# Optimization experiments

Hardware: AMD Instinct MI355X
Metric: run time of the kernel (lower is better)

Reference implementation:

```python
import jax, jax.numpy as jnp
import numpy as np

LAYERS, STACKS, K = 10, 3, 2
DILATIONS = [2 ** i for _ in range(STACKS) for i in range(LAYERS)]  # 30 layers


def conv1d(x, w, b=None, dilation=1):
    # x: [N, C_in, T], w: [C_out, C_in, K] (torch Conv1d layout), VALID padding
    out = jax.lax.conv_general_dilated(
        x, w, window_strides=(1,), padding='VALID',
        rhs_dilation=(dilation,), dimension_numbers=('NCH', 'OIH', 'NCH'))
    if b is not None:
        out = out + b[None, :, None]
    return out


def setup_inputs() -> dict:
    key = jax.random.key(0)
    ks = jax.random.split(key, 12)
    s = 0.1  # weight scale to avoid gate saturation
    return {
        'y': jax.random.normal(ks[0], (16, 1, 16384), dtype=jnp.float32),
        'causal_w': jax.random.normal(ks[1], (32, 1, 1), dtype=jnp.float32) * s,
        'causal_b': jax.random.normal(ks[2], (32,), dtype=jnp.float32) * s,
        'filt_w': jax.random.normal(ks[3], (30, 32, 32, K), dtype=jnp.float32) * s,
        'gate_w': jax.random.normal(ks[4], (30, 32, 32, K), dtype=jnp.float32) * s,
        'res_w': jax.random.normal(ks[5], (30, 32, 32, 1), dtype=jnp.float32) * s,
        'skip_w': jax.random.normal(ks[6], (30, 256, 32, 1), dtype=jnp.float32) * s,
        'end1_w': jax.random.normal(ks[7], (256, 256, 1), dtype=jnp.float32) * s,
        'end1_b': jax.random.normal(ks[8], (256,), dtype=jnp.float32) * s,
        'end2_w': jax.random.normal(ks[9], (256, 256, 1), dtype=jnp.float32) * s,
        'end2_b': jax.random.normal(ks[10], (256,), dtype=jnp.float32) * s,
    }


def reference(y, causal_w, causal_b, filt_w, gate_w, res_w, skip_w,
              end1_w, end1_b, end2_w, end2_b):
    x = conv1d(y, causal_w, causal_b)  # [B, 32, T]
    skip = None
    for i, d in enumerate(DILATIONS):
        r = x
        f = jnp.tanh(conv1d(x, filt_w[i], dilation=d))      # [B,32,T-d]
        g = jax.nn.sigmoid(conv1d(x, gate_w[i], dilation=d))
        x = f * g
        s = conv1d(x, skip_w[i])                             # [B,256,T-d]
        t = s.shape[-1]
        skip = s if skip is None else s + skip[:, :, -t:]
        x = conv1d(x, res_w[i])
        x = x + r[:, :, -x.shape[-1]:]
    x = jax.nn.relu(skip)
    x = jax.nn.relu(conv1d(x, end1_w, end1_b))
    x = conv1d(x, end2_w, end2_b)
    return x
```

## Files before the change

kernel.cpp:

```cpp
#include <hip/hip_runtime.h>
#include <hip/hip_bf16.h>
#include <cstdint>

#define NB 16
#define NC 32
#define T0 16384
#define NL 30
#define SKC 256
#define TF 13315
#define WGRP 192
#define XBC 320
#define XBS 20

typedef _Float16 f16;
typedef _Float16 f16x2 __attribute__((ext_vector_type(2)));
typedef _Float16 f16x8 __attribute__((ext_vector_type(8)));
typedef float f32x4 __attribute__((ext_vector_type(4)));
typedef uint32_t u32;

#define MFMA16(a,b,c) __builtin_amdgcn_mfma_f32_16x16x32_f16(a,b,c,0,0,0)

#define SCF (-2.88539008f)
#define SCG (-1.44269504f)
#define CLF 86.6f
#define CLG 43.3f

__device__ __forceinline__ float frcp(float x){
#if __has_builtin(__builtin_amdgcn_rcpf)
  return __builtin_amdgcn_rcpf(x);
#else
  return 1.f/x;
#endif
}
__device__ __forceinline__ float fexp2(float x){
#if __has_builtin(__builtin_amdgcn_exp2f)
  return __builtin_amdgcn_exp2f(x);
#else
  return exp2f(x);
#endif
}
__device__ __forceinline__ float clampf(float x, float c){
#if __has_builtin(__builtin_amdgcn_fmed3f)
  return __builtin_amdgcn_fmed3f(x, -c, c);
#else
  return fminf(fmaxf(x, -c), c);
#endif
}
__device__ __forceinline__ u32 pk2(float x, float y){
#if __has_builtin(__builtin_amdgcn_cvt_pkrtz)
  return __builtin_bit_cast(u32, __builtin_amdgcn_cvt_pkrtz(x, y));
#else
  f16x2 r; r.x = (f16)x; r.y = (f16)y;
  return __builtin_bit_cast(u32, r);
#endif
}
__device__ __forceinline__ u32 pkadd(u32 a, u32 b){
  f16x2 s = __builtin_bit_cast(f16x2, a) + __builtin_bit_cast(f16x2, b);
  return __builtin_bit_cast(u32, s);
}
__device__ __forceinline__ size_t zfrag_off(int lz, int q){
  return (size_t)(lz & ~63)*NC + (size_t)(((lz>>4)&3)*512 + (q*16 + (lz&15))*8);
}
__device__ __forceinline__ int sigma_co(int q, int j){
  return (j < 4) ? (4*q + j) : (12 + 4*q + j);
}

__global__ __launch_bounds__(256) void prep3(
    const float* __restrict__ sw, const float* __restrict__ e1w,
    const float* __restrict__ e2w, const float* __restrict__ fw,
    const float* __restrict__ gw, const float* __restrict__ rw,
    f16* __restrict__ wsk, f16* __restrict__ e1f, f16* __restrict__ e2f,
    f16* __restrict__ fgpf, f16* __restrict__ ggpf, u32* __restrict__ rwp){
  int idx = blockIdx.x*256 + threadIdx.x;
  if (idx < 30720){
    int lane = idx & 63, mt = (idx>>6)&15, i = idx>>10;
    int m = mt*16 + (lane&15);
    int q = lane >> 4;
    const float* s = sw + ((size_t)i*SKC + m)*NC;
    f16* dp = wsk + (size_t)idx*8;
    #pragma unroll
    for (int j=0;j<8;j++) dp[j] = (f16)s[sigma_co(q, j)];
  } else if (idx < 38912){
    int j2 = idx - 30720;
    int lane = j2&63, mt = (j2>>6)&15, ks = j2>>10;
    int m = mt*16 + (lane&15);
    int k = ks*32 + (lane>>4)*8;
    const float* s = e1w + (size_t)m*SKC + k;
    f16* dp = e1f + (size_t)j2*8;
    #pragma unroll
    for (int j=0;j<8;j++) dp[j] = (f16)s[j];
  } else if (idx < 47104){
    int j2 = idx - 38912;
    int lane = j2&63, mt = (j2>>6)&15, ks = j2>>10;
    int m = mt*16 + (lane&15);
    int k = ks*32 + (lane>>4)*8;
    const float* s = e2w + (size_t)m*SKC + k;
    f16* dp = e2f + (size_t)j2*8;
    #pragma unroll
    for (int j=0;j<8;j++) dp[j] = (f16)s[j];
  } else if (idx < 77824){
    int j2 = idx - 47104;
    const float* s = fw + (size_t)j2*2;
    size_t base = (size_t)(j2 >> 5) * 64;
    int ci = j2 & 31;
    fgpf[base + ci]      = (f16)(s[0]*SCF);
    fgpf[base + 32 + ci] = (f16)(s[1]*SCF);
  } else if (idx < 108544){
    int j2 = idx - 77824;
    const float* s = gw + (size_t)j2*2;
    size_t base = (size_t)(j2 >> 5) * 64;
    int ci = j2 & 31;
    ggpf[base + ci]      = (f16)(s[0]*SCG);
    ggpf[base + 32 + ci] = (f16)(s[1]*SCG);
  } else if (idx < 123904){
    int j2 = idx - 108544;
    int i = j2 >> 9, c = (j2>>4)&31, pj = j2&15;
    const float* s = rw + ((size_t)i*NC + c)*NC;
    int q = pj >> 2, j0 = (2*pj) & 7;
    int c0 = sigma_co(q, j0);
    f16x2 p; p.x = (f16)s[c0]; p.y = (f16)s[c0+1];
    rwp[j2] = __builtin_bit_cast(u32, p);
  }
}

struct LW { f16x8 af[4]; f16x8 ag[4]; f16x8 ar[2]; };
__device__ __forceinline__ void lw_load(LW& w, const f16* __restrict__ fp,
    const f16* __restrict__ gp, const u32* __restrict__ rp, int lane){
  int m = lane & 15, q8 = (lane >> 4) * 8, q4 = (lane >> 4) * 4;
  #pragma unroll
  for (int mh = 0; mh < 2; mh++){
    #pragma unroll
    for (int tap = 0; tap < 2; tap++){
      w.af[mh*2+tap] = *(const f16x8*)&fp[((mh*16+m)*2+tap)*32 + q8];
      w.ag[mh*2+tap] = *(const f16x8*)&gp[((mh*16+m)*2+tap)*32 + q8];
    }
    w.ar[mh] = *(const f16x8*)&rp[(mh*16+m)*16 + q4];
  }
}

__device__ __forceinline__ void tile_core(const LW& w,
    uint4 a, uint4 b, uint2 rb0, uint2 rb1,
    uint4& zfrag, uint2& xo0, uint2& xo1){
  f16x8 A  = __builtin_bit_cast(f16x8, a);
  f16x8 Bt = __builtin_bit_cast(f16x8, b);
  f32x4 z4 = {0.f,0.f,0.f,0.f};
  f32x4 fa0 = MFMA16(w.af[0], A, z4); fa0 = MFMA16(w.af[1], Bt, fa0);
  f32x4 fa1 = MFMA16(w.af[2], A, z4); fa1 = MFMA16(w.af[3], Bt, fa1);
  f32x4 ga0 = MFMA16(w.ag[0], A, z4); ga0 = MFMA16(w.ag[1], Bt, ga0);
  f32x4 ga1 = MFMA16(w.ag[2], A, z4); ga1 = MFMA16(w.ag[3], Bt, ga1);
  u32 zq[4];
  #pragma unroll
  for (int mh = 0; mh < 2; mh++){
    f32x4 fv = mh ? fa1 : fa0;
    f32x4 gv = mh ? ga1 : ga0;
    float zz[4];
    #pragma unroll
    for (int r = 0; r < 4; r++){
      float t = fexp2(clampf(fv[r], CLF));
      float u = fexp2(clampf(gv[r], CLG));
      zz[r] = (1.f - t) * frcp((1.f + t) * (1.f + u));
    }
    zq[mh*2+0] = pk2(zz[0], zz[1]);
    zq[mh*2+1] = pk2(zz[2], zz[3]);
  }
  zfrag = make_uint4(zq[0], zq[1], zq[2], zq[3]);
  f16x8 zB = __builtin_bit_cast(f16x8, zfrag);
  f32x4 r0 = MFMA16(w.ar[0], zB, z4);
  f32x4 r1 = MFMA16(w.ar[1], zB, z4);
  xo0.x = pkadd(pk2(r0[0], r0[1]), rb0.x);
  xo0.y = pkadd(pk2(r0[2], r0[3]), rb0.y);
  xo1.x = pkadd(pk2(r1[0], r1[1]), rb1.x);
  xo1.y = pkadd(pk2(r1[2], r1[3]), rb1.y);
}

struct Trim7 { int t[7]; };

__global__ __launch_bounds__(256, 3) void group7m(
    const f16* __restrict__ xin, const float* __restrict__ y,
    const float* __restrict__ cw, const float* __restrict__ cb, int tc0,
    f16* __restrict__ xout, f16* __restrict__ zbase, int g0,
    int Lfinal, int TcAct, int zrows, int xpb,
    const f16* __restrict__ fgpf, const f16* __restrict__ ggpf,
    const u32* __restrict__ rwp, Trim7 trims){
  __shared__ u32 xb[2][XBC*XBS];
  int tid = threadIdx.x, b = blockIdx.y, o0 = blockIdx.x*WGRP;
  int lane = tid & 63, widx = tid >> 6;
  int Cf = Lfinal - o0; if (Cf > WGRP) Cf = WGRP;
  int Cin = Cf + 127;
  for (int p = tid; p < Cin; p += 256){
    u32* dst = &xb[0][p*XBS];
    if (y != nullptr){
      float yv = y[(size_t)b*T0 + tc0 + o0 + p];
      #pragma unroll
      for (int j = 0; j < 16; j++)
        dst[j] = pk2(fmaf(cw[2*j], yv, cb[2*j]), fmaf(cw[2*j+1], yv, cb[2*j+1]));
    } else {
      const uint4* src = (const uint4*)(xin + ((size_t)b*xpb + o0 + p)*NC);
      uint4* d4 = (uint4*)dst;
      d4[0]=src[0]; d4[1]=src[1]; d4[2]=src[2]; d4[3]=src[3];
    }
  }
  __syncthreads();
  int cur = 0;
  int tl = lane & 15, q = lane >> 4;
  size_t zlayer = (size_t)512*zrows;
  LW w;
  lw_load(w, fgpf + (size_t)g0*2048, ggpf + (size_t)g0*2048,
          rwp + (size_t)g0*512, lane);
  #pragma unroll 1
  for (int li = 0; li < 7; li++){
    int d = 1 << li;
    int count = Cf + 128 - (2 << li);
    LW wn;
    if (li < 6)
      lw_load(wn, fgpf + (size_t)(g0+li+1)*2048, ggpf + (size_t)(g0+li+1)*2048,
              rwp + (size_t)(g0+li+1)*512, lane);
    f16* zl = zbase + (size_t)(g0+li)*zlayer + (size_t)b*zrows*NC;
    int trim = trims.t[li];
    int ntiles = (count + 15) >> 4;
    for (int ti = widx; ti < ntiles; ti += 4){
      int c = ti*16 + tl;
      const u32* xc = &xb[cur][c*XBS];
      const u32* xd = &xb[cur][(c+d)*XBS];
      uint4 a  = *(const uint4*)&xc[q*4];
      uint4 b4 = *(const uint4*)&xd[q*4];
      uint2 rb0 = *(const uint2*)&xd[q*2];
      uint2 rb1 = *(const uint2*)&xd[8 + q*2];
      uint4 zf; uint2 xo0, xo1;
      tile_core(w, a, b4, rb0, rb1, zf, xo0, xo1);
      u32* xn = &xb[cur^1][c*XBS];
      *(uint2*)&xn[q*2] = xo0;
      *(uint2*)&xn[8 + q*2] = xo1;
      int lz = o0 + c - trim;
      if (c < count && lz >= 0 && lz < TcAct)
        *(uint4*)(zl + zfrag_off(lz, q)) = zf;
    }
    __syncthreads();
    if (li < 6) w = wn;
    cur ^= 1;
  }
  for (int p = tid; p < Cf; p += 256){
    const uint4* s4 = (const uint4*)&xb[cur][p*XBS];
    uint4* dd = (uint4*)(xout + ((size_t)b*xpb + o0 + p)*NC);
    dd[0]=s4[0]; dd[1]=s4[1]; dd[2]=s4[2]; dd[3]=s4[3];
  }
}

__global__ __launch_bounds__(256, 3) void singlem(
    const f16* __restrict__ xin, f16* __restrict__ xout, f16* __restrict__ zl,
    const f16* __restrict__ fp, const f16* __restrict__ gp,
    const u32* __restrict__ rp, int Tout, int d, int trim, int TcAct,
    int zrows, int xpb){
  int tid = threadIdx.x, b = blockIdx.y;
  int lane = tid & 63, widx = tid >> 6;
  int t0A = (blockIdx.x*8 + widx*2) * 16;
  if (t0A >= Tout) return;
  int haveB = (t0A + 16) < Tout;
  LW w;
  lw_load(w, fp, gp, rp, lane);
  int tl = lane & 15, q = lane >> 4;
  const f16* xbase = xin + (size_t)b*xpb*NC;
  int cA = t0A + tl;
  const f16* xcA = xbase + (size_t)cA*NC;
  const f16* xdA = xcA + (size_t)d*NC;
  uint4 aA  = *(const uint4*)(xcA + q*8);
  uint4 bA  = *(const uint4*)(xdA + q*8);
  uint2 r0A = *(const uint2*)(xdA + q*4);
  uint2 r1A = *(const uint2*)(xdA + 16 + q*4);
  int cB = cA + 16;
  const f16* xcB = xbase + (size_t)cB*NC;
  const f16* xdB = xcB + (size_t)d*NC;
  uint4 aB  = *(const uint4*)(xcB + q*8);
  uint4 bB  = *(const uint4*)(xdB + q*8);
  uint2 r0B = *(const uint2*)(xdB + q*4);
  uint2 r1B = *(const uint2*)(xdB + 16 + q*4);

  uint4 zfA, zfB; uint2 xo0A, xo1A, xo0B, xo1B;
  tile_core(w, aA, bA, r0A, r1A, zfA, xo0A, xo1A);
  tile_core(w, aB, bB, r0B, r1B, zfB, xo0B, xo1B);

  if (cA < Tout){
    f16* xoc = xout + ((size_t)b*xpb + cA)*NC;
    *(uint2*)(xoc + q*4) = xo0A;
    *(uint2*)(xoc + 16 + q*4) = xo1A;
  }
  if (haveB && cB < Tout){
    f16* xoc = xout + ((size_t)b*xpb + cB)*NC;
    *(uint2*)(xoc + q*4) = xo0B;
    *(uint2*)(xoc + 16 + q*4) = xo1B;
  }
  f16* zlb = zl + (size_t)b*zrows*NC;
  {
    int lz = cA - trim;
    if (cA < Tout && lz >= 0 && lz < TcAct)
      *(uint4*)(zlb + zfrag_off(lz, q)) = zfA;
  }
  if (haveB){
    int lz = cB - trim;
    if (cB < Tout && lz >= 0 && lz < TcAct)
      *(uint4*)(zlb + zfrag_off(lz, q)) = zfB;
  }
}

__global__ __launch_bounds__(256, 4) void skipend(
    const f16* __restrict__ zbase,
    const f16* __restrict__ wsk, const f16* __restrict__ e1f,
    const float* __restrict__ e1b, const f16* __restrict__ e2f,
    const float* __restrict__ e2b, float* __restrict__ out,
    int tc0, int TcAct, int zrows){
  __shared__ u32 smem[64*132];
  int tid = threadIdx.x, b = blockIdx.y, t0 = blockIdx.x*64;
  int w = tid>>6, lane = tid&63;
  int tl = lane & 15;
  int q  = lane >> 4;
  const uint4* wsk4 = (const uint4*)wsk;
  const uint4* e1f4 = (const uint4*)e1f;
  const uint4* e2f4 = (const uint4*)e2f;
  const uint4* zsrc = (const uint4*)(zbase + ((size_t)b*zrows + t0)*NC) + tid;
  size_t zstep4 = (size_t)64*zrows;

  f32x4 acc[4][4];
  #pragma unroll
  for (int j=0;j<4;j++)
    #pragma unroll
    for (int tt=0;tt<4;tt++) acc[j][tt] = f32x4{0.f,0.f,0.f,0.f};

  uint4* ring = (uint4*)smem;
  uint4 pz0, pz1, pz2;
  pz0 = zsrc[0]; pz1 = zsrc[zstep4]; pz2 = zsrc[2*zstep4];
  ring[tid] = pz0; ring[256 + tid] = pz1; ring[512 + tid] = pz2;
  pz0 = zsrc[3*zstep4]; pz1 = zsrc[4*zstep4]; pz2 = zsrc[5*zstep4];
  __syncthreads();

  #pragma unroll 1
  for (int g = 0; g < 10; g++){
    const uint4* zr = (const uint4*)smem + (g&1)*768;
    int lbase = g*3;
    #pragma unroll
    for (int k = 0; k < 3; k++){
      uint4 aw0 = wsk4[(size_t)(lbase+k)*1024 + (w*4+0)*64 + lane];
      uint4 aw1 = wsk4[(size_t)(lbase+k)*1024 + (w*4+1)*64 + lane];
      uint4 aw2 = wsk4[(size_t)(lbase+k)*1024 + (w*4+2)*64 + lane];
      uint4 aw3 = wsk4[(size_t)(lbase+k)*1024 + (w*4+3)*64 + lane];
      f16x8 zb0 = *(const f16x8*)&zr[k*256 + 0*64 + lane];
      f16x8 zb1 = *(const f16x8*)&zr[k*256 + 1*64 + lane];
      f16x8 zb2 = *(const f16x8*)&zr[k*256 + 2*64 + lane];
      f16x8 zb3 = *(const f16x8*)&zr[k*256 + 3*64 + lane];
      f16x8 a0 = __builtin_bit_cast(f16x8, aw0);
      f16x8 a1 = __builtin_bit_cast(f16x8, aw1);
      f16x8 a2 = __builtin_bit_cast(f16x8, aw2);
      f16x8 a3 = __builtin_bit_cast(f16x8, aw3);
      acc[0][0] = MFMA16(a0, zb0, acc[0][0]);
      acc[0][1] = MFMA16(a0, zb1, acc[0][1]);
      acc[0][2] = MFMA16(a0, zb2, acc[0][2]);
      acc[0][3] = MFMA16(a0, zb3, acc[0][3]);
      acc[1][0] = MFMA16(a1, zb0, acc[1][0]);
      acc[1][1] = MFMA16(a1, zb1, acc[1][1]);
      acc[1][2] = MFMA16(a1, zb2, acc[1][2]);
      acc[1][3] = MFMA16(a1, zb3, acc[1][3]);
      acc[2][0] = MFMA16(a2, zb0, acc[2][0]);
      acc[2][1] = MFMA16(a2, zb1, acc[2][1]);
      acc[2][2] = MFMA16(a2, zb2, acc[2][2]);
      acc[2][3] = MFMA16(a2, zb3, acc[2][3]);
      acc[3][0] = MFMA16(a3, zb0, acc[3][0]);
      acc[3][1] = MFMA16(a3, zb1, acc[3][1]);
      acc[3][2] = MFMA16(a3, zb2, acc[3][2]);
      acc[3][3] = MFMA16(a3, zb3, acc[3][3]);
    }
    if (g < 9){
      uint4* wr = (uint4*)smem + ((g+1)&1)*768;
      wr[tid] = pz0; wr[256 + tid] = pz1; wr[512 + tid] = pz2;
      if (g < 8){
        size_t nb = (size_t)(3*(g+2))*zstep4;
        pz0 = zsrc[nb]; pz1 = zsrc[nb + zstep4]; pz2 = zsrc[nb + 2*zstep4];
      }
      __syncthreads();
    }
  }
  __syncthreads();
  int rq = q*4;
  #pragma unroll
  for (int j=0;j<4;j++){
    int c0 = (w*4+j)*16 + rq;
    #pragma unroll
    for (int tt=0;tt<4;tt++){
      int t = tt*16 + tl;
      u32 p0 = pk2(fmaxf(acc[j][tt][0],0.f), fmaxf(acc[j][tt][1],0.f));
      u32 p1 = pk2(fmaxf(acc[j][tt][2],0.f), fmaxf(acc[j][tt][3],0.f));
      *(uint2*)&smem[t*132 + (c0>>1)] = make_uint2(p0, p1);
    }
  }
  __syncthreads();
  #pragma unroll
  for (int j=0;j<4;j++)
    #pragma unroll
    for (int tt=0;tt<4;tt++) acc[j][tt] = f32x4{0.f,0.f,0.f,0.f};
  #pragma unroll
  for (int ks=0;ks<8;ks++){
    f16x8 zb[4];
    #pragma unroll
    for (int tt=0;tt<4;tt++)
      zb[tt] = *(const f16x8*)&smem[(tt*16+tl)*132 + ks*16 + q*4];
    #pragma unroll
    for (int j=0;j<4;j++){
      f16x8 a = __builtin_bit_cast(f16x8, e1f4[(size_t)(ks*16 + w*4+j)*64 + lane]);
      #pragma unroll
      for (int tt=0;tt<4;tt++)
        acc[j][tt] = MFMA16(a, zb[tt], acc[j][tt]);
    }
  }
  __syncthreads();
  #pragma unroll
  for (int j=0;j<4;j++){
    int c0 = (w*4+j)*16 + rq;
    float4 bv = *(const float4*)&e1b[c0];
    #pragma unroll
    for (int tt=0;tt<4;tt++){
      int t = tt*16 + tl;
      u32 p0 = pk2(fmaxf(acc[j][tt][0]+bv.x,0.f), fmaxf(acc[j][tt][1]+bv.y,0.f));
      u32 p1 = pk2(fmaxf(acc[j][tt][2]+bv.z,0.f), fmaxf(acc[j][tt][3]+bv.w,0.f));
      *(uint2*)&smem[t*132 + (c0>>1)] = make_uint2(p0, p1);
    }
  }
  __syncthreads();
  #pragma unroll
  for (int j=0;j<4;j++)
    #pragma unroll
    for (int tt=0;tt<4;tt++) acc[j][tt] = f32x4{0.f,0.f,0.f,0.f};
  #pragma unroll
  for (int ks=0;ks<8;ks++){
    f16x8 zb[4];
    #pragma unroll
    for (int tt=0;tt<4;tt++)
      zb[tt] = *(const f16x8*)&smem[(tt*16+tl)*132 + ks*16 + q*4];
    #pragma unroll
    for (int j=0;j<4;j++){
      f16x8 a = __builtin_bit_cast(f16x8, e2f4[(size_t)(ks*16 + w*4+j)*64 + lane]);
      #pragma unroll
      for (int tt=0;tt<4;tt++)
        acc[j][tt] = MFMA16(a, zb[tt], acc[j][tt]);
    }
  }
  #pragma unroll
  for (int j=0;j<4;j++){
    int c0 = (w*4+j)*16 + rq;
    float4 bv = *(const float4*)&e2b[c0];
    #pragma unroll
    for (int tt=0;tt<4;tt++){
      int t = tt*16 + tl;
      if (t0 + t < TcAct){
        float* op = out + ((size_t)b*SKC + c0)*TF + tc0 + t0 + t;
        op[0*TF] = acc[j][tt][0] + bv.x;
        op[1*TF] = acc[j][tt][1] + bv.y;
        op[2*TF] = acc[j][tt][2] + bv.z;
        op[3*TF] = acc[j][tt][3] + bv.w;
      }
    }
  }
}

extern "C" void kernel_launch(void* const* d_in, const int* in_sizes, int n_in,
                              void* d_out, int out_size, void* d_ws, size_t ws_size,
                              hipStream_t stream) {
  (void)in_sizes; (void)n_in; (void)out_size;
  const float* y   = (const float*)d_in[0];
  const float* cw  = (const float*)d_in[1];
  const float* cb  = (const float*)d_in[2];
  const float* fw  = (const float*)d_in[3];
  const float* gw  = (const float*)d_in[4];
  const float* rw  = (const float*)d_in[5];
  const float* sw  = (const float*)d_in[6];
  const float* e1w = (const float*)d_in[7];
  const float* e1b = (const float*)d_in[8];
  const float* e2w = (const float*)d_in[9];
  const float* e2b = (const float*)d_in[10];
  float* out = (float*)d_out;
  char* ws = (char*)d_ws;

  const size_t fixedW = 1060864;
  int TCc = 0, xpb = 0;
  for (int c = 1; c <= 6; c++){
    int tcc = (((TF + c - 1)/c) + 63) & ~63;
    int xp  = tcc + 3264;
    size_t need = fixedW + 2*(size_t)xp*1024 + (size_t)NL*512*(size_t)tcc*2;
    if (need <= ws_size){ TCc = tcc; xpb = xp; break; }
  }
  if (!TCc){ TCc = 2240; xpb = 2240 + 3264; }

  f16* wsk   = (f16*)(ws);
  f16* e1f   = (f16*)(ws +   491520);
  f16* e2f   = (f16*)(ws +   622592);
  f16* fgpf  = (f16*)(ws +  753664);
  f16* ggpf  = (f16*)(ws +  876544);
  u32* rwp   = (u32*)(ws +  999424);
  f16* xpA   = (f16*)(ws + fixedW);
  f16* xpB   = (f16*)(ws + fixedW + (size_t)xpb*1024);
  f16* zstack = (f16*)(ws + fixedW + 2*(size_t)xpb*1024);

  int S[NL+1]; S[NL] = 0;
  for (int i = NL-1; i >= 0; i--) S[i] = S[i+1] + (1 << (i % 10));

  prep3<<<dim3(484), 256, 0, stream>>>(sw, e1w, e2w, fw, gw, rw,
                                       wsk, e1f, e2f, fgpf, ggpf, rwp);

  f16* bufs[2] = {xpA, xpB};
  for (int tc0 = 0; tc0 < TF; tc0 += TCc){
    int TcAct = TF - tc0; if (TcAct > TCc) TcAct = TCc;
    int cur = 0;
    for (int s = 0; s < 3; s++){
      int g0 = s*10;
      Trim7 tr;
      for (int li = 0; li < 7; li++) tr.t[li] = S[g0+li+1];
      int Lfinal = TcAct + S[g0+7];
      const f16* gin = (s == 0) ? (const f16*)nullptr : bufs[cur];
      const float* yArg = (s == 0) ? y : (const float*)nullptr;
      int nxt = (s == 0) ? 0 : (cur ^ 1);
      group7m<<<dim3((Lfinal + WGRP-1)/WGRP, NB), 256, 0, stream>>>(
          gin, yArg, cw, cb, tc0, bufs[nxt], zstack, g0, Lfinal, TcAct,
          TCc, xpb, fgpf, ggpf, rwp, tr);
      cur = nxt;
      for (int i = g0+7; i <= g0+9; i++){
        int d = 1 << (i % 10);
        int Tout = TcAct + S[i+1];
        singlem<<<dim3((Tout + 127)/128, NB), 256, 0, stream>>>(
            bufs[cur], bufs[cur^1], zstack + (size_t)i*512*TCc,
            fgpf + (size_t)i*2048, ggpf + (size_t)i*2048, rwp + (size_t)i*512,
            Tout, d, S[i+1], TcAct, TCc, xpb);
        cur ^= 1;
      }
    }
    skipend<<<dim3((TcAct + 63)/64, NB), 256, 0, stream>>>(
        zstack, wsk, e1f, e1b, e2f, e2b, out, tc0, TcAct, TCc);
  }
}
```

Measured before the change: 717.4 us.

## Use 512-thread skipend blocks with direct global-to-LDS async staging of z

The skipend kernel now runs 8 waves per block instead of 4, and each wave computes 2 output-channel tiles instead of 4, which halves the accumulator registers per thread. The z fragments are staged into the LDS double buffer with global_load_lds (direct global-to-LDS copies) when the builtin exists, replacing the register-prefetch ring. The next group's load is issued before the MFMAs on the current buffer, so the copy is meant to overlap compute without holding staged data in registers. The trade-off is more waves per block and a barrier after every group, and correctness relies on the async LDS writes having completed by that barrier.

New measurement: 657.5 us, median of 4. 1.09x faster.

```diff
diff --git a/kernel.cpp b/kernel.cpp
--- a/kernel.cpp
+++ b/kernel.cpp
@@ -58,6 +58,16 @@
   f16x2 s = __builtin_bit_cast(f16x2, a) + __builtin_bit_cast(f16x2, b);
   return __builtin_bit_cast(u32, s);
 }
+#if __has_builtin(__builtin_amdgcn_global_load_lds)
+#define HAVE_GLL 1
+__device__ __forceinline__ void gll16(const void* g, void* l){
+  __builtin_amdgcn_global_load_lds(
+      (const __attribute__((address_space(1))) u32*)g,
+      (__attribute__((address_space(3))) u32*)l, 16, 0, 0);
+}
+#else
+#define HAVE_GLL 0
+#endif
 __device__ __forceinline__ size_t zfrag_off(int lz, int q){
   return (size_t)(lz & ~63)*NC + (size_t)(((lz>>4)&3)*512 + (q*16 + (lz&15))*8);
 }
@@ -302,7 +312,7 @@
   }
 }
 
-__global__ __launch_bounds__(256, 4) void skipend(
+__global__ __launch_bounds__(512, 2) void skipend(
     const f16* __restrict__ zbase,
     const f16* __restrict__ wsk, const f16* __restrict__ e1f,
     const float* __restrict__ e1b, const f16* __restrict__ e2f,
@@ -316,40 +326,47 @@
   const uint4* wsk4 = (const uint4*)wsk;
   const uint4* e1f4 = (const uint4*)e1f;
   const uint4* e2f4 = (const uint4*)e2f;
-  const uint4* zsrc = (const uint4*)(zbase + ((size_t)b*zrows + t0)*NC) + tid;
-  size_t zstep4 = (size_t)64*zrows;
-
-  f32x4 acc[4][4];
-  #pragma unroll
-  for (int j=0;j<4;j++)
+  size_t zstepf = (size_t)512*zrows;
+  const f16* zsrcb = zbase + ((size_t)b*zrows + t0)*NC;
+
+  f32x4 acc[2][4];
+  #pragma unroll
+  for (int j=0;j<2;j++)
     #pragma unroll
     for (int tt=0;tt<4;tt++) acc[j][tt] = f32x4{0.f,0.f,0.f,0.f};
 
-  uint4* ring = (uint4*)smem;
-  uint4 pz0, pz1, pz2;
-  pz0 = zsrc[0]; pz1 = zsrc[zstep4]; pz2 = zsrc[2*zstep4];
-  ring[tid] = pz0; ring[256 + tid] = pz1; ring[512 + tid] = pz2;
-  pz0 = zsrc[3*zstep4]; pz1 = zsrc[4*zstep4]; pz2 = zsrc[5*zstep4];
+  auto stage = [&](int half, int lbase){
+    #pragma unroll 1
+    for (int s = w; s < 12; s += 8){
+      int ks = s>>2, sq = s&3;
+#if HAVE_GLL
+      gll16(zsrcb + (size_t)(lbase+ks)*zstepf + (size_t)(sq*64+lane)*8,
+            smem + (size_t)half*3072 + ks*1024 + sq*256);
+#else
+      uint4 v = *(const uint4*)(zsrcb + (size_t)(lbase+ks)*zstepf +
+                                (size_t)(sq*64+lane)*8);
+      *(uint4*)(smem + (size_t)half*3072 + ks*1024 + sq*256 + lane*4) = v;
+#endif
+    }
+  };
+
+  stage(0, 0);
   __syncthreads();
-
   #pragma unroll 1
   for (int g = 0; g < 10; g++){
-    const uint4* zr = (const uint4*)smem + (g&1)*768;
+    if (g < 9) stage((g+1)&1, 3*(g+1));
+    const uint4* zr = (const uint4*)(smem + (size_t)(g&1)*3072);
     int lbase = g*3;
     #pragma unroll
     for (int k = 0; k < 3; k++){
-      uint4 aw0 = wsk4[(size_t)(lbase+k)*1024 + (w*4+0)*64 + lane];
-      uint4 aw1 = wsk4[(size_t)(lbase+k)*1024 + (w*4+1)*64 + lane];
-      uint4 aw2 = wsk4[(size_t)(lbase+k)*1024 + (w*4+2)*64 + lane];
-      uint4 aw3 = wsk4[(size_t)(lbase+k)*1024 + (w*4+3)*64 + lane];
+      uint4 aw0 = wsk4[(size_t)(lbase+k)*1024 + (w*2+0)*64 + lane];
+      uint4 aw1 = wsk4[(size_t)(lbase+k)*1024 + (w*2+1)*64 + lane];
       f16x8 zb0 = *(const f16x8*)&zr[k*256 + 0*64 + lane];
       f16x8 zb1 = *(const f16x8*)&zr[k*256 + 1*64 + lane];
       f16x8 zb2 = *(const f16x8*)&zr[k*256 + 2*64 + lane];
       f16x8 zb3 = *(const f16x8*)&zr[k*256 + 3*64 + lane];
       f16x8 a0 = __builtin_bit_cast(f16x8, aw0);
       f16x8 a1 = __builtin_bit_cast(f16x8, aw1);
-      f16x8 a2 = __builtin_bit_cast(f16x8, aw2);
-      f16x8 a3 = __builtin_bit_cast(f16x8, aw3);
       acc[0][0] = MFMA16(a0, zb0, acc[0][0]);
       acc[0][1] = MFMA16(a0, zb1, acc[0][1]);
       acc[0][2] = MFMA16(a0, zb2, acc[0][2]);
@@ -358,30 +375,13 @@
       acc[1][1] = MFMA16(a1, zb1, acc[1][1]);
       acc[1][2] = MFMA16(a1, zb2, acc[1][2]);
       acc[1][3] = MFMA16(a1, zb3, acc[1][3]);
-      acc[2][0] = MFMA16(a2, zb0, acc[2][0]);
-      acc[2][1] = MFMA16(a2, zb1, acc[2][1]);
-      acc[2][2] = MFMA16(a2, zb2, acc[2][2]);
-      acc[2][3] = MFMA16(a2, zb3, acc[2][3]);
-      acc[3][0] = MFMA16(a3, zb0, acc[3][0]);
-      acc[3][1] = MFMA16(a3, zb1, acc[3][1]);
-      acc[3][2] = MFMA16(a3, zb2, acc[3][2]);
-      acc[3][3] = MFMA16(a3, zb3, acc[3][3]);
-    }
-    if (g < 9){
-      uint4* wr = (uint4*)smem + ((g+1)&1)*768;
-      wr[tid] = pz0; wr[256 + tid] = pz1; wr[512 + tid] = pz2;
-      if (g < 8){
-        size_t nb = (size_t)(3*(g+2))*zstep4;
-        pz0 = zsrc[nb]; pz1 = zsrc[nb + zstep4]; pz2 = zsrc[nb + 2*zstep4];
-      }
-      __syncthreads();
-    }
-  }
-  __syncthreads();
+    }
+    __syncthreads();
+  }
   int rq = q*4;
   #pragma unroll
-  for (int j=0;j<4;j++){
-    int c0 = (w*4+j)*16 + rq;
+  for (int j=0;j<2;j++){
+    int c0 = (w*2+j)*16 + rq;
     #pragma unroll
     for (int tt=0;tt<4;tt++){
       int t = tt*16 + tl;
@@ -392,7 +392,7 @@
   }
   __syncthreads();
   #pragma unroll
-  for (int j=0;j<4;j++)
+  for (int j=0;j<2;j++)
     #pragma unroll
     for (int tt=0;tt<4;tt++) acc[j][tt] = f32x4{0.f,0.f,0.f,0.f};
   #pragma unroll
@@ -402,8 +402,8 @@
     for (int tt=0;tt<4;tt++)
       zb[tt] = *(const f16x8*)&smem[(tt*16+tl)*132 + ks*16 + q*4];
     #pragma unroll
-    for (int j=0;j<4;j++){
-      f16x8 a = __builtin_bit_cast(f16x8, e1f4[(size_t)(ks*16 + w*4+j)*64 + lane]);
+    for (int j=0;j<2;j++){
+      f16x8 a = __builtin_bit_cast(f16x8, e1f4[(size_t)(ks*16 + w*2+j)*64 + lane]);
       #pragma unroll
       for (int tt=0;tt<4;tt++)
         acc[j][tt] = MFMA16(a, zb[tt], acc[j][tt]);
@@ -411,8 +411,8 @@
   }
   __syncthreads();
   #pragma unroll
-  for (int j=0;j<4;j++){
-    int c0 = (w*4+j)*16 + rq;
+  for (int j=0;j<2;j++){
+    int c0 = (w*2+j)*16 + rq;
     float4 bv = *(const float4*)&e1b[c0];
     #pragma unroll
     for (int tt=0;tt<4;tt++){
@@ -424,7 +424,7 @@
   }
   __syncthreads();
   #pragma unroll
-  for (int j=0;j<4;j++)
+  for (int j=0;j<2;j++)
     #pragma unroll
     for (int tt=0;tt<4;tt++) acc[j][tt] = f32x4{0.f,0.f,0.f,0.f};
   #pragma unroll
@@ -434,16 +434,16 @@
     for (int tt=0;tt<4;tt++)
       zb[tt] = *(const f16x8*)&smem[(tt*16+tl)*132 + ks*16 + q*4];
     #pragma unroll
-    for (int j=0;j<4;j++){
-      f16x8 a = __builtin_bit_cast(f16x8, e2f4[(size_t)(ks*16 + w*4+j)*64 + lane]);
+    for (int j=0;j<2;j++){
+      f16x8 a = __builtin_bit_cast(f16x8, e2f4[(size_t)(ks*16 + w*2+j)*64 + lane]);
       #pragma unroll
       for (int tt=0;tt<4;tt++)
         acc[j][tt] = MFMA16(a, zb[tt], acc[j][tt]);
     }
   }
   #pragma unroll
-  for (int j=0;j<4;j++){
-    int c0 = (w*4+j)*16 + rq;
+  for (int j=0;j<2;j++){
+    int c0 = (w*2+j)*16 + rq;
     float4 bv = *(const float4*)&e2b[c0];
     #pragma unroll
     for (int tt=0;tt<4;tt++){
@@ -529,7 +529,7 @@
         cur ^= 1;
       }
     }
-    skipend<<<dim3((TcAct + 63)/64, NB), 256, 0, stream>>>(
+    skipend<<<dim3((TcAct + 63)/64, NB), 512, 0, stream>>>(
         zstack, wsk, e1f, e1b, e2f, e2b, out, tc0, TcAct, TCc);
   }
 }
```
